# Optimization experiments

Measured on AMD Instinct MI355X. Metric: run time of the kernel, lower is better.

Reference implementation:

```python
import jax, jax.numpy as jnp
import numpy as np

N = 100000   # nodes
E = 3200000  # edges (avg degree 32)
F_IN = 128   # node feature dim (lazy in_channels)
C = 16       # GAT out_channels, heads=1
ED = 2       # edge_dim
B = 512      # graphs in batch
OUT_X = 64; OUT_Y = 64; ROT = 4
EPS = 1e-5


def _bn(x, g, b):
    # BatchNorm1d in training mode: biased batch variance, eps=1e-5
    mu = x.mean(0, keepdims=True)
    var = x.var(0, keepdims=True)
    return g * (x - mu) * jax.lax.rsqrt(var + EPS) + b


def _gat(x, src, dst, edge_attr, W, We, att_s, att_d, att_e, bias):
    # PyG GATConv, heads=1: self-loops added with fill_value='mean' edge attrs
    n = x.shape[0]
    deg = jax.ops.segment_sum(jnp.ones_like(dst, jnp.float32), dst, num_segments=n)
    loop_attr = jax.ops.segment_sum(edge_attr, dst, num_segments=n) / jnp.maximum(deg, 1.0)[:, None]
    idx = jnp.arange(n)
    src_f = jnp.concatenate([src, idx])
    dst_f = jnp.concatenate([dst, idx])
    ea = jnp.concatenate([edge_attr, loop_attr], axis=0)  # [E+N, ED]
    h = x @ W                      # [N, C]
    a_s = h @ att_s                # [N]
    a_d = h @ att_d                # [N]
    a_e = (ea @ We) @ att_e        # [E+N]
    logits = jax.nn.leaky_relu(a_s[src_f] + a_d[dst_f] + a_e, 0.2)
    m = jax.ops.segment_max(logits, dst_f, num_segments=n)  # every node has a self-loop
    ex = jnp.exp(logits - m[dst_f])
    alpha = ex / jax.ops.segment_sum(ex, dst_f, num_segments=n)[dst_f]
    return jax.ops.segment_sum(alpha[:, None] * h[src_f], dst_f, num_segments=n) + bias


def _glorot(k, shp):
    lim = float(np.sqrt(6.0 / (shp[0] + shp[1])))
    return jax.random.uniform(k, shp, jnp.float32, -lim, lim)


def setup_inputs() -> dict:
    key = jax.random.key(0)
    k = jax.random.split(key, 48)
    d = {}
    d['x'] = jax.random.normal(k[0], (N, F_IN), jnp.float32)
    d['edge_index'] = jax.random.randint(k[1], (2, E), 0, N)
    d['edge_attr'] = jax.random.normal(k[2], (E, ED), jnp.float32)
    d['batch'] = jnp.sort(jax.random.randint(k[3], (N,), 0, B))
    # gat1
    d['W1'] = _glorot(k[4], (F_IN, C)); d['We1'] = _glorot(k[5], (ED, C))
    d['as1'] = 0.1 * jax.random.normal(k[6], (C,)); d['ad1'] = 0.1 * jax.random.normal(k[7], (C,))
    d['ae1'] = 0.1 * jax.random.normal(k[8], (C,)); d['b1'] = jnp.zeros((C,), jnp.float32)
    # norm1 (BatchNorm on nodes)
    d['g1'] = 1.0 + 0.1 * jax.random.normal(k[9], (C,)); d['bb1'] = 0.1 * jax.random.normal(k[10], (C,))
    # gat2
    d['W2'] = _glorot(k[11], (C, C)); d['We2'] = _glorot(k[12], (ED, C))
    d['as2'] = 0.1 * jax.random.normal(k[13], (C,)); d['ad2'] = 0.1 * jax.random.normal(k[14], (C,))
    d['ae2'] = 0.1 * jax.random.normal(k[15], (C,)); d['b2'] = jnp.zeros((C,), jnp.float32)
    # D2RL MLP tail
    d['gL1'] = 1.0 + 0.1 * jax.random.normal(k[16], (C,)); d['bL1'] = 0.1 * jax.random.normal(k[17], (C,))
    d['Wl1'] = _glorot(k[18], (C, C)); d['bl1'] = 0.1 * jax.random.normal(k[19], (C,))
    d['gL2'] = 1.0 + 0.1 * jax.random.normal(k[20], (2 * C,)); d['bL2'] = 0.1 * jax.random.normal(k[21], (2 * C,))
    d['Wl2'] = _glorot(k[22], (2 * C, C)); d['bl2'] = 0.1 * jax.random.normal(k[23], (C,))
    d['gL3'] = 1.0 + 0.1 * jax.random.normal(k[24], (2 * C,)); d['bL3'] = 0.1 * jax.random.normal(k[25], (2 * C,))
    d['Wl3'] = _glorot(k[26], (2 * C, C)); d['bl3'] = 0.1 * jax.random.normal(k[27], (C,))
    d['Wx'] = _glorot(k[28], (C, OUT_X)); d['bx'] = 0.1 * jax.random.normal(k[29], (OUT_X,))
    d['Wy'] = _glorot(k[30], (C, OUT_Y)); d['by'] = 0.1 * jax.random.normal(k[31], (OUT_Y,))
    d['Wr'] = _glorot(k[32], (C, ROT)); d['br'] = 0.1 * jax.random.normal(k[33], (ROT,))
    return d


def reference(x, edge_index, edge_attr, batch,
              W1, We1, as1, ad1, ae1, b1, g1, bb1,
              W2, We2, as2, ad2, ae2, b2,
              gL1, bL1, Wl1, bl1, gL2, bL2, Wl2, bl2, gL3, bL3, Wl3, bl3,
              Wx, bx, Wy, by, Wr, br):
    src, dst = edge_index[0], edge_index[1]
    h = jax.nn.relu(_gat(x, src, dst, edge_attr, W1, We1, as1, ad1, ae1, b1))
    h = _bn(h, g1, bb1)
    h = jax.nn.relu(_gat(h, src, dst, edge_attr, W2, We2, as2, ad2, ae2, b2))
    # MeanAggregation over graphs
    cnt = jax.ops.segment_sum(jnp.ones((h.shape[0],), jnp.float32), batch, num_segments=B)
    xe = jax.ops.segment_sum(h, batch, num_segments=B) / jnp.maximum(cnt, 1.0)[:, None]  # [B, C]
    z = _bn(xe, gL1, bL1)
    z = jax.nn.relu(z @ Wl1 + bl1)
    z = _bn(jnp.concatenate([z, xe], axis=1), gL2, bL2)
    z = jax.nn.relu(z @ Wl2 + bl2)
    z = _bn(jnp.concatenate([z, xe], axis=1), gL3, bL3)
    z = jax.nn.relu(z @ Wl3 + bl3)
    xx = jax.nn.softmax(z @ Wx + bx, axis=1)
    y = jax.nn.softmax(z @ Wy + by, axis=1)
    rot = jax.nn.softmax(z @ Wr + br, axis=1)
    return (xx, y, rot)
```

## Files before the change

kernel.cpp:

```cpp
#include <hip/hip_runtime.h>
#include <hip/hip_fp16.h>
#include <math.h>

#define C 16
#define FIN 128

typedef unsigned int u32x2 __attribute__((ext_vector_type(2)));

__global__ __launch_bounds__(256) void k_gemm1(
    const float* __restrict__ x, const float* __restrict__ W,
    const float* __restrict__ asw, const float* __restrict__ adw,
    __half* __restrict__ hh, float* __restrict__ a_s, float* __restrict__ a_d, int n) {
  __shared__ float xs[64 * 129];
  __shared__ float Ws[FIN * C];
  __shared__ float pAs[4][64], pAd[4][64];
  int t = threadIdx.x;
  int node0 = blockIdx.x * 64;
  for (int i = t; i < FIN * C; i += 256) Ws[i] = W[i];
  for (int i = t; i < 64 * FIN; i += 256) {
    int r = i >> 7, c = i & 127;
    int node = node0 + r;
    xs[r * 129 + c] = (node < n) ? x[(size_t)node * FIN + c] : 0.f;
  }
  __syncthreads();
  int nn = t & 63, cg = (t >> 6) * 4, grp = t >> 6;
  float a0 = 0.f, a1 = 0.f, a2 = 0.f, a3 = 0.f;
  const float* xr = &xs[nn * 129];
  #pragma unroll 8
  for (int k = 0; k < FIN; ++k) {
    float xv = xr[k];
    const float* wr = &Ws[k * C + cg];
    a0 += xv * wr[0]; a1 += xv * wr[1]; a2 += xv * wr[2]; a3 += xv * wr[3];
  }
  int node = node0 + nn;
  if (node < n) {
    __half2 p0 = __floats2half2_rn(a0, a1), p1 = __floats2half2_rn(a2, a3);
    unsigned u0, u1;
    memcpy(&u0, &p0, 4); memcpy(&u1, &p1, 4);
    *(uint2*)(hh + (size_t)node * 16 + cg) = make_uint2(u0, u1);
  }
  pAs[grp][nn] = a0 * asw[cg] + a1 * asw[cg + 1] + a2 * asw[cg + 2] + a3 * asw[cg + 3];
  pAd[grp][nn] = a0 * adw[cg] + a1 * adw[cg + 1] + a2 * adw[cg + 2] + a3 * adw[cg + 3];
  __syncthreads();
  if (t < 64 && node0 + t < n) {
    a_s[node0 + t] = pAs[0][t] + pAs[1][t] + pAs[2][t] + pAs[3][t];
    a_d[node0 + t] = pAd[0][t] + pAd[1][t] + pAd[2][t] + pAd[3][t];
  }
}

__global__ __launch_bounds__(512) void k_scan1(const int* __restrict__ counts,
                                               int* __restrict__ bsum, int n) {
  __shared__ int sd[512];
  int i = blockIdx.x * 512 + threadIdx.x;
  sd[threadIdx.x] = (i < n) ? counts[i] : 0;
  __syncthreads();
  for (int s = 256; s > 0; s >>= 1) {
    if (threadIdx.x < s) sd[threadIdx.x] += sd[threadIdx.x + s];
    __syncthreads();
  }
  if (threadIdx.x == 0) bsum[blockIdx.x] = sd[0];
}

__global__ __launch_bounds__(512) void k_scan2(int* __restrict__ bsum,
                                               int* __restrict__ offs,
                                               int nblk, int n) {
  __shared__ int sd[512];
  int t = threadIdx.x;
  int v = (t < nblk) ? bsum[t] : 0;
  sd[t] = v;
  __syncthreads();
  for (int off = 1; off < 512; off <<= 1) {
    int x = (t >= off) ? sd[t - off] : 0;
    __syncthreads();
    sd[t] += x;
    __syncthreads();
  }
  if (t < nblk) bsum[t] = sd[t] - v;
  if (t == nblk - 1) offs[n] = sd[t];
}

__global__ __launch_bounds__(512) void k_scan3(const int* __restrict__ counts,
                                               const int* __restrict__ bsum,
                                               int* __restrict__ offs, int n) {
  __shared__ int sd[512];
  int t = threadIdx.x;
  int i = blockIdx.x * 512 + t;
  int v = (i < n) ? counts[i] : 0;
  sd[t] = v;
  __syncthreads();
  for (int off = 1; off < 512; off <<= 1) {
    int x = (t >= off) ? sd[t - off] : 0;
    __syncthreads();
    sd[t] += x;
    __syncthreads();
  }
  if (i < n) offs[i] = bsum[blockIdx.x] + sd[t] - v;
}


__global__ __launch_bounds__(256) void k_p1count(
    const int* __restrict__ dst, int* __restrict__ histT,
    int ne, int chunk, int G, int nbin) {
  __shared__ int hist[512];
  int g = blockIdx.x, t = threadIdx.x;
  for (int i = t; i < nbin; i += 256) hist[i] = 0;
  __syncthreads();
  int e0 = g * chunk, e1 = e0 + chunk; if (e1 > ne) e1 = ne;
  for (int e = e0 + t; e < e1; e += 256) atomicAdd(&hist[dst[e] >> 8], 1);
  __syncthreads();
  for (int i = t; i < nbin; i += 256) histT[i * G + g] = hist[i];
}

__global__ __launch_bounds__(256) void k_p1scat(
    const int* __restrict__ src, const int* __restrict__ dst,
    const float2* __restrict__ ea, const int* __restrict__ histS,
    const float* __restrict__ We1, const float* __restrict__ ae1,
    const float* __restrict__ We2, const float* __restrict__ ae2,
    uint2* __restrict__ tmpR, int* __restrict__ tmpD,
    int ne, int chunk, int G, int nbin) {
  __shared__ int cur[512];
  int g = blockIdx.x, t = threadIdx.x;
  for (int i = t; i < nbin; i += 256) cur[i] = histS[i * G + g];
  float w01 = 0.f, w11 = 0.f, w02 = 0.f, w12 = 0.f;
  #pragma unroll
  for (int c = 0; c < C; ++c) {
    w01 += We1[c] * ae1[c]; w11 += We1[C + c] * ae1[c];
    w02 += We2[c] * ae2[c]; w12 += We2[C + c] * ae2[c];
  }
  __syncthreads();
  int e0 = g * chunk, e1 = e0 + chunk; if (e1 > ne) e1 = ne;
  for (int e = e0 + t; e < e1; e += 256) {
    int d = dst[e];
    int pos = atomicAdd(&cur[d >> 8], 1);
    float2 a = ea[e];
    __half2 hp = __floats2half2_rn(a.x * w01 + a.y * w11, a.x * w02 + a.y * w12);
    unsigned hb;
    memcpy(&hb, &hp, 4);
    tmpR[pos] = make_uint2((unsigned)src[e], hb);
    tmpD[pos] = d;
  }
}

__global__ __launch_bounds__(256) void k_p2(
    const uint2* __restrict__ tmpR, const int* __restrict__ tmpD,
    const int* __restrict__ histS,
    uint2* __restrict__ bucket, int* __restrict__ offs,
    int G, int nbin, int n, int ne) {
  __shared__ int hist[256], scn[256], cur[256];
  int b = blockIdx.x, t = threadIdx.x;
  int cs0 = histS[b * G];
  int cs1 = (b + 1 < nbin) ? histS[(b + 1) * G] : ne;
  hist[t] = 0;
  __syncthreads();
  for (int i = cs0 + t; i < cs1; i += 256) atomicAdd(&hist[tmpD[i] & 255], 1);
  __syncthreads();
  int v = hist[t];
  scn[t] = v;
  __syncthreads();
  for (int off = 1; off < 256; off <<= 1) {
    int x = (t >= off) ? scn[t - off] : 0;
    __syncthreads();
    scn[t] += x;
    __syncthreads();
  }
  int excl = scn[t] - v;
  int node = b * 256 + t;
  if (node <= n) offs[node] = cs0 + excl;
  if (b == 0 && t == 0) offs[n] = ne;
  cur[t] = cs0 + excl;
  __syncthreads();
  for (int i = cs0 + t; i < cs1; i += 256) {
    int d = tmpD[i];
    int pos = atomicAdd(&cur[d & 255], 1);
    bucket[pos] = tmpR[i];
  }
}

__global__ __launch_bounds__(256) void k_hist_rank(
    const int* __restrict__ dst, int* __restrict__ counts,
    int* __restrict__ rank, int ne) {
  int e = blockIdx.x * 256 + threadIdx.x;
  if (e < ne) rank[e] = atomicAdd(&counts[dst[e]], 1);
}

__global__ __launch_bounds__(256) void k_scatter(
    const int* __restrict__ src, const int* __restrict__ dst,
    const float2* __restrict__ ea, const int* __restrict__ offs,
    const int* __restrict__ rank,
    const float* __restrict__ We1, const float* __restrict__ ae1,
    const float* __restrict__ We2, const float* __restrict__ ae2,
    uint2* __restrict__ bucket, int ne) {
  int e = blockIdx.x * 256 + threadIdx.x;
  if (e >= ne) return;
  float w01 = 0.f, w11 = 0.f, w02 = 0.f, w12 = 0.f;
  #pragma unroll
  for (int c = 0; c < C; ++c) {
    w01 += We1[c] * ae1[c]; w11 += We1[C + c] * ae1[c];
    w02 += We2[c] * ae2[c]; w12 += We2[C + c] * ae2[c];
  }
  int d = dst[e];
  float2 a = ea[e];
  __half2 hp = __floats2half2_rn(a.x * w01 + a.y * w11, a.x * w02 + a.y * w12);
  unsigned hb;
  memcpy(&hb, &hp, 4);
  bucket[offs[d] + rank[e]] = make_uint2((unsigned)src[e], hb);
}

__global__ __launch_bounds__(256) void k_gather(
    const uint2* __restrict__ bucket, const int* __restrict__ offs,
    const float* __restrict__ a_s, const float* __restrict__ a_d,
    const __half* __restrict__ hh, const float* __restrict__ bias,
    float* __restrict__ outv, float* __restrict__ bnsum, float* __restrict__ bnsq,
    int lay, int do_bn, int n) {
  __shared__ float sbn[32];
  int t = threadIdx.x;
  if (do_bn) {
    if (t < 32) sbn[t] = 0.f;
    __syncthreads();
  }

  int node = blockIdx.x * 64 + (t >> 2);
  int l = t & 3, f = l & 1, p = l >> 1;

  float acc[8];
  #pragma unroll
  for (int j = 0; j < 8; ++j) acc[j] = 0.f;
  float den = 0.f, ssum = 0.f;
  int o0 = 0, o1 = 0;
  float adi = 0.f, asi = 0.f;
  if (node < n) {
    o0 = offs[node]; o1 = offs[node + 1];
    adi = a_d[node]; asi = a_s[node];
    int e = o0 + p;
    u32x2 r = {0u, 0u};
    if (e < o1) r = __builtin_nontemporal_load((const u32x2*)(bucket + e));
    while (e < o1) {
      int en = e + 2;
      u32x2 rn = {0u, 0u};
      if (en < o1) rn = __builtin_nontemporal_load((const u32x2*)(bucket + en));
      int s = (int)r.x;
      unsigned scb = r.y;
      __half2 sc2;
      memcpy(&sc2, &scb, 4);
      float se = lay ? __high2float(sc2) : __low2float(sc2);
      float asv = a_s[s];
      uint4 hv = *(const uint4*)(hh + ((size_t)s << 4) + (f << 3));
      float lg = asv + adi + se;
      lg = lg > 0.f ? lg : 0.2f * lg;
      float ex = __expf(lg);
      den += ex; ssum += se;
      __half2 t0, t1, t2, t3;
      memcpy(&t0, &hv.x, 4); memcpy(&t1, &hv.y, 4);
      memcpy(&t2, &hv.z, 4); memcpy(&t3, &hv.w, 4);
      float2 g0 = __half22float2(t0), g1 = __half22float2(t1);
      float2 g2 = __half22float2(t2), g3 = __half22float2(t3);
      acc[0] += ex * g0.x; acc[1] += ex * g0.y;
      acc[2] += ex * g1.x; acc[3] += ex * g1.y;
      acc[4] += ex * g2.x; acc[5] += ex * g2.y;
      acc[6] += ex * g3.x; acc[7] += ex * g3.y;
      r = rn; e = en;
    }
  }
  den += __shfl_xor(den, 2);
  ssum += __shfl_xor(ssum, 2);
  #pragma unroll
  for (int j = 0; j < 8; ++j) acc[j] += __shfl_xor(acc[j], 2);

  float v[8];
  #pragma unroll
  for (int j = 0; j < 8; ++j) v[j] = 0.f;
  if (node < n) {
    float dgc = fmaxf((float)(o1 - o0), 1.f);
    float lg = asi + adi + ssum / dgc;
    lg = lg > 0.f ? lg : 0.2f * lg;
    float exs = __expf(lg);
    uint4 hv = *(const uint4*)(hh + ((size_t)node << 4) + (f << 3));
    __half2 t0, t1, t2, t3;
    memcpy(&t0, &hv.x, 4); memcpy(&t1, &hv.y, 4);
    memcpy(&t2, &hv.z, 4); memcpy(&t3, &hv.w, 4);
    float2 g0 = __half22float2(t0), g1 = __half22float2(t1);
    float2 g2 = __half22float2(t2), g3 = __half22float2(t3);
    float hs[8] = {g0.x, g0.y, g1.x, g1.y, g2.x, g2.y, g3.x, g3.y};
    float inv = 1.f / (den + exs);
    const float* bp = bias + f * 8;
    #pragma unroll
    for (int j = 0; j < 8; ++j)
      v[j] = fmaxf((acc[j] + exs * hs[j]) * inv + bp[j], 0.f);
    if (p == 0) {
      float4* op = (float4*)(outv + ((size_t)node << 4));
      op[f * 2]     = make_float4(v[0], v[1], v[2], v[3]);
      op[f * 2 + 1] = make_float4(v[4], v[5], v[6], v[7]);
    }
  }

  if (do_bn) {
    float sv[8], qv[8];
    bool act = (node < n) && (p == 0);
    #pragma unroll
    for (int j = 0; j < 8; ++j) {
      sv[j] = act ? v[j] : 0.f;
      qv[j] = sv[j] * sv[j];
    }
    #pragma unroll
    for (int j = 0; j < 8; ++j) {
      sv[j] += __shfl_down(sv[j], 4);  qv[j] += __shfl_down(qv[j], 4);
      sv[j] += __shfl_down(sv[j], 8);  qv[j] += __shfl_down(qv[j], 8);
      sv[j] += __shfl_down(sv[j], 16); qv[j] += __shfl_down(qv[j], 16);
      sv[j] += __shfl_down(sv[j], 32); qv[j] += __shfl_down(qv[j], 32);
    }
    if ((t & 63) < 2) {
      #pragma unroll
      for (int j = 0; j < 8; ++j) {
        atomicAdd(&sbn[f * 8 + j], sv[j]);
        atomicAdd(&sbn[16 + f * 8 + j], qv[j]);
      }
    }
    __syncthreads();
    if (t < 16) atomicAdd(&bnsum[t], sbn[t]);
    else if (t < 32) atomicAdd(&bnsq[t - 16], sbn[t]);
  }
}

__global__ void k_bnp(const float* __restrict__ bnsum, const float* __restrict__ bnsq,
                      const float* __restrict__ g, const float* __restrict__ bb,
                      float* __restrict__ scale, float* __restrict__ shift, float invn) {
  int c = threadIdx.x;
  if (c >= C) return;
  float mean = bnsum[c] * invn;
  float var = bnsq[c] * invn - mean * mean;
  float s = g[c] * rsqrtf(var + 1e-5f);
  scale[c] = s; shift[c] = bb[c] - mean * s;
}

__global__ __launch_bounds__(256) void k_node2(
    const float* __restrict__ outv, const float* __restrict__ scale,
    const float* __restrict__ shift, const float* __restrict__ W2,
    const float* __restrict__ asw, const float* __restrict__ adw,
    __half* __restrict__ hh, float* __restrict__ a_s, float* __restrict__ a_d, int n) {
  __shared__ float w2s[C * C];
  if (threadIdx.x < C * C) w2s[threadIdx.x] = W2[threadIdx.x];
  __syncthreads();
  int i = blockIdx.x * 256 + threadIdx.x;
  if (i >= n) return;
  float hn[C];
  #pragma unroll
  for (int c = 0; c < C; ++c) hn[c] = outv[(size_t)i * C + c] * scale[c] + shift[c];
  float h2[C];
  #pragma unroll
  for (int j = 0; j < C; ++j) {
    float acc = 0.f;
    #pragma unroll
    for (int c = 0; c < C; ++c) acc += hn[c] * w2s[c * C + j];
    h2[j] = acc;
  }
  float hs = 0.f, hd = 0.f;
  #pragma unroll
  for (int j = 0; j < C; ++j) { hs += h2[j] * asw[j]; hd += h2[j] * adw[j]; }
  a_s[i] = hs; a_d[i] = hd;
  unsigned wbits[8];
  #pragma unroll
  for (int j = 0; j < 8; ++j) {
    __half2 hq = __floats2half2_rn(h2[2 * j], h2[2 * j + 1]);
    memcpy(&wbits[j], &hq, 4);
  }
  uint4* hp = (uint4*)(hh + (size_t)i * 16);
  hp[0] = make_uint4(wbits[0], wbits[1], wbits[2], wbits[3]);
  hp[1] = make_uint4(wbits[4], wbits[5], wbits[6], wbits[7]);
}

__global__ void k_gstart(const int* __restrict__ batch, int* __restrict__ gs,
                         int n, int B_) {
  int g = blockIdx.x * blockDim.x + threadIdx.x;
  if (g > B_) return;
  if (g == B_) { gs[B_] = n; return; }
  int lo = 0, hi = n;
  while (lo < hi) { int mid = (lo + hi) >> 1; if (batch[mid] < g) lo = mid + 1; else hi = mid; }
  gs[g] = lo;
}

__global__ __launch_bounds__(256) void k_xe(
    const float* __restrict__ outv, const int* __restrict__ gs,
    float* __restrict__ xe, int B_) {
  int wave = blockIdx.x * 4 + (threadIdx.x >> 6);
  if (wave >= B_) return;
  int lane = threadIdx.x & 63;
  int c = lane & 15, sub = lane >> 4;
  int base = gs[wave], end = gs[wave + 1];
  float s = 0.f;
  for (int n0 = base + sub; n0 < end; n0 += 4) s += outv[(size_t)n0 * C + c];
  s += __shfl_down(s, 32);
  s += __shfl_down(s, 16);
  if (lane < 16) xe[(size_t)wave * C + c] = s / fmaxf((float)(end - base), 1.f);
}

__global__ __launch_bounds__(512) void k_tail_z3(
    const float* __restrict__ xe_in,
    const float* __restrict__ gL1, const float* __restrict__ bL1,
    const float* __restrict__ Wl1, const float* __restrict__ bl1,
    const float* __restrict__ gL2, const float* __restrict__ bL2,
    const float* __restrict__ Wl2, const float* __restrict__ bl2,
    const float* __restrict__ gL3, const float* __restrict__ bL3,
    const float* __restrict__ Wl3, const float* __restrict__ bl3,
    float* __restrict__ z3buf, int B_) {
  __shared__ float ssum[2 * C], ssq[2 * C], sc[2 * C], sh[2 * C];
  int t = threadIdx.x;
  float invB = 1.f / (float)B_;
  float xe[C];
  #pragma unroll
  for (int c = 0; c < C; ++c) xe[c] = xe_in[(size_t)t * C + c];

  if (t < 2 * C) { ssum[t] = 0.f; ssq[t] = 0.f; }
  __syncthreads();
  #pragma unroll
  for (int c = 0; c < C; ++c) {
    float s = xe[c], q = xe[c] * xe[c];
    for (int o = 32; o > 0; o >>= 1) { s += __shfl_down(s, o); q += __shfl_down(q, o); }
    if ((t & 63) == 0) { atomicAdd(&ssum[c], s); atomicAdd(&ssq[c], q); }
  }
  __syncthreads();
  if (t < C) {
    float mean = ssum[t] * invB, var = ssq[t] * invB - mean * mean;
    float s = gL1[t] * rsqrtf(var + 1e-5f);
    sc[t] = s; sh[t] = bL1[t] - mean * s;
  }
  __syncthreads();
  float z[C];
  #pragma unroll
  for (int j = 0; j < C; ++j) {
    float acc = bl1[j];
    #pragma unroll
    for (int c = 0; c < C; ++c) acc += (xe[c] * sc[c] + sh[c]) * Wl1[c * C + j];
    z[j] = fmaxf(acc, 0.f);
  }
  __syncthreads();

  if (t < 2 * C) { ssum[t] = 0.f; ssq[t] = 0.f; }
  __syncthreads();
  #pragma unroll
  for (int c = 0; c < C; ++c) {
    float s = z[c], q = z[c] * z[c];
    for (int o = 32; o > 0; o >>= 1) { s += __shfl_down(s, o); q += __shfl_down(q, o); }
    if ((t & 63) == 0) { atomicAdd(&ssum[c], s); atomicAdd(&ssq[c], q); }
    float s2 = xe[c], q2 = xe[c] * xe[c];
    for (int o = 32; o > 0; o >>= 1) { s2 += __shfl_down(s2, o); q2 += __shfl_down(q2, o); }
    if ((t & 63) == 0) { atomicAdd(&ssum[C + c], s2); atomicAdd(&ssq[C + c], q2); }
  }
  __syncthreads();
  if (t < 2 * C) {
    float mean = ssum[t] * invB, var = ssq[t] * invB - mean * mean;
    float s = gL2[t] * rsqrtf(var + 1e-5f);
    sc[t] = s; sh[t] = bL2[t] - mean * s;
  }
  __syncthreads();
  float z2[C];
  #pragma unroll
  for (int j = 0; j < C; ++j) {
    float acc = bl2[j];
    #pragma unroll
    for (int c = 0; c < C; ++c) acc += (z[c] * sc[c] + sh[c]) * Wl2[c * C + j];
    #pragma unroll
    for (int c = 0; c < C; ++c) acc += (xe[c] * sc[C + c] + sh[C + c]) * Wl2[(C + c) * C + j];
    z2[j] = fmaxf(acc, 0.f);
  }
  __syncthreads();

  if (t < 2 * C) { ssum[t] = 0.f; ssq[t] = 0.f; }
  __syncthreads();
  #pragma unroll
  for (int c = 0; c < C; ++c) {
    float s = z2[c], q = z2[c] * z2[c];
    for (int o = 32; o > 0; o >>= 1) { s += __shfl_down(s, o); q += __shfl_down(q, o); }
    if ((t & 63) == 0) { atomicAdd(&ssum[c], s); atomicAdd(&ssq[c], q); }
    float s2 = xe[c], q2 = xe[c] * xe[c];
    for (int o = 32; o > 0; o >>= 1) { s2 += __shfl_down(s2, o); q2 += __shfl_down(q2, o); }
    if ((t & 63) == 0) { atomicAdd(&ssum[C + c], s2); atomicAdd(&ssq[C + c], q2); }
  }
  __syncthreads();
  if (t < 2 * C) {
    float mean = ssum[t] * invB, var = ssq[t] * invB - mean * mean;
    float s = gL3[t] * rsqrtf(var + 1e-5f);
    sc[t] = s; sh[t] = bL3[t] - mean * s;
  }
  __syncthreads();
  #pragma unroll
  for (int j = 0; j < C; ++j) {
    float acc = bl3[j];
    #pragma unroll
    for (int c = 0; c < C; ++c) acc += (z2[c] * sc[c] + sh[c]) * Wl3[c * C + j];
    #pragma unroll
    for (int c = 0; c < C; ++c) acc += (xe[c] * sc[C + c] + sh[C + c]) * Wl3[(C + c) * C + j];
    z3buf[(size_t)t * C + j] = fmaxf(acc, 0.f);
  }
}

__global__ __launch_bounds__(256) void k_heads(
    const float* __restrict__ z3buf,
    const float* __restrict__ Wx, const float* __restrict__ bx,
    const float* __restrict__ Wy, const float* __restrict__ by,
    const float* __restrict__ Wr, const float* __restrict__ br,
    float* __restrict__ out, int B_) {
  int wv = blockIdx.x * 4 + (threadIdx.x >> 6);
  if (wv >= B_) return;
  int lane = threadIdx.x & 63;
  float z[C];
  #pragma unroll
  for (int c = 0; c < C; ++c) z[c] = z3buf[(size_t)wv * C + c];

  float ax = bx[lane];
  #pragma unroll
  for (int c = 0; c < C; ++c) ax += z[c] * Wx[c * 64 + lane];
  float m = ax;
  #pragma unroll
  for (int o = 32; o > 0; o >>= 1) m = fmaxf(m, __shfl_xor(m, o));
  float e = __expf(ax - m);
  float s = e;
  #pragma unroll
  for (int o = 32; o > 0; o >>= 1) s += __shfl_xor(s, o);
  out[(size_t)wv * 64 + lane] = e / s;

  float ay = by[lane];
  #pragma unroll
  for (int c = 0; c < C; ++c) ay += z[c] * Wy[c * 64 + lane];
  m = ay;
  #pragma unroll
  for (int o = 32; o > 0; o >>= 1) m = fmaxf(m, __shfl_xor(m, o));
  e = __expf(ay - m);
  s = e;
  #pragma unroll
  for (int o = 32; o > 0; o >>= 1) s += __shfl_xor(s, o);
  out[(size_t)B_ * 64 + (size_t)wv * 64 + lane] = e / s;

  if (lane < 4) {
    float ar = br[lane];
    #pragma unroll
    for (int c = 0; c < C; ++c) ar += z[c] * Wr[c * 4 + lane];
    float mr = ar;
    mr = fmaxf(mr, __shfl_xor(mr, 1));
    mr = fmaxf(mr, __shfl_xor(mr, 2));
    float er = __expf(ar - mr);
    float sr = er;
    sr += __shfl_xor(sr, 1);
    sr += __shfl_xor(sr, 2);
    out[(size_t)B_ * 128 + (size_t)wv * 4 + lane] = er / sr;
  }
}

extern "C" void kernel_launch(void* const* d_in, const int* in_sizes, int n_in,
                              void* d_out, int out_size, void* d_ws, size_t ws_size,
                              hipStream_t stream) {
  const float* x     = (const float*)d_in[0];
  const int*   eidx  = (const int*)d_in[1];
  const float* eattr = (const float*)d_in[2];
  const int*   batch = (const int*)d_in[3];
  const float* W1  = (const float*)d_in[4];
  const float* We1 = (const float*)d_in[5];
  const float* as1 = (const float*)d_in[6];
  const float* ad1 = (const float*)d_in[7];
  const float* ae1 = (const float*)d_in[8];
  const float* b1  = (const float*)d_in[9];
  const float* g1  = (const float*)d_in[10];
  const float* bb1 = (const float*)d_in[11];
  const float* W2  = (const float*)d_in[12];
  const float* We2 = (const float*)d_in[13];
  const float* as2 = (const float*)d_in[14];
  const float* ad2 = (const float*)d_in[15];
  const float* ae2 = (const float*)d_in[16];
  const float* b2  = (const float*)d_in[17];
  const float* gL1 = (const float*)d_in[18];
  const float* bL1 = (const float*)d_in[19];
  const float* Wl1 = (const float*)d_in[20];
  const float* bl1 = (const float*)d_in[21];
  const float* gL2 = (const float*)d_in[22];
  const float* bL2 = (const float*)d_in[23];
  const float* Wl2 = (const float*)d_in[24];
  const float* bl2 = (const float*)d_in[25];
  const float* gL3 = (const float*)d_in[26];
  const float* bL3 = (const float*)d_in[27];
  const float* Wl3 = (const float*)d_in[28];
  const float* bl3 = (const float*)d_in[29];
  const float* Wx  = (const float*)d_in[30];
  const float* bx  = (const float*)d_in[31];
  const float* Wy  = (const float*)d_in[32];
  const float* by  = (const float*)d_in[33];
  const float* Wr  = (const float*)d_in[34];
  const float* br  = (const float*)d_in[35];

  int N = in_sizes[3];
  int E = in_sizes[2] / 2;
  int B = out_size / 132;

  const int* src = eidx;
  const int* dst = eidx + E;

  const int G = 256;
  int nbin = (N + 255) >> 8;
  int nscan = nbin * G;
  int chunk = (E + G - 1) / G;
  int nblk2 = (nscan + 511) / 512;

  char* w = (char*)d_ws;
  size_t o = 0;
  auto alloc = [&](size_t bytes) { char* p = w + o; o += (bytes + 15) & ~15ull; return p; };
  uint2*  bucket = (uint2*)alloc((size_t)E * 8);
  uint2*  tmpR   = (uint2*)alloc((size_t)E * 8);
  int*    tmpD   = (int*)alloc((size_t)E * 4);
  __half* hh     = (__half*)alloc((size_t)N * C * 2);
  float*  outv   = (float*)alloc((size_t)N * C * 4);
  float*  a_s    = (float*)alloc((size_t)N * 4);
  float*  a_d    = (float*)alloc((size_t)N * 4);
  int*    offs   = (int*)alloc((size_t)(N + 4) * 4);
  int*    histT  = (int*)alloc((size_t)(nscan + 4) * 4);
  int*    histS  = (int*)alloc((size_t)(nscan + 4) * 4);
  int*    bsum   = (int*)alloc((size_t)(nblk2 + 516) * 4);
  float*  bn     = (float*)alloc(64 * 4);
  float*  xe     = (float*)alloc((size_t)B * C * 4);
  int*    gs     = (int*)alloc((size_t)(B + 4) * 4);
  float*  z3buf  = (float*)alloc((size_t)B * C * 4);
  size_t need_radix = o;

  bool radix = (need_radix <= ws_size) && (nbin <= 512) && (nblk2 <= 512);

  hipMemsetAsync(bn, 0, 32 * 4, stream);
  k_gemm1<<<(N + 63) / 64, 256, 0, stream>>>(x, W1, as1, ad1, hh, a_s, a_d, N);

  if (radix) {
    k_p1count<<<G, 256, 0, stream>>>(dst, histT, E, chunk, G, nbin);
    k_scan1<<<nblk2, 512, 0, stream>>>(histT, bsum, nscan);
    k_scan2<<<1, 512, 0, stream>>>(bsum, histS, nblk2, nscan);
    k_scan3<<<nblk2, 512, 0, stream>>>(histT, bsum, histS, nscan);
    k_p1scat<<<G, 256, 0, stream>>>(src, dst, (const float2*)eattr, histS,
                                    We1, ae1, We2, ae2, tmpR, tmpD, E, chunk, G, nbin);
    k_p2<<<nbin, 256, 0, stream>>>(tmpR, tmpD, histS, bucket, offs, G, nbin, N, E);
  } else {
    int* rank   = (int*)tmpR;
    int* counts = (int*)tmpD;
    int nblk = (N + 511) / 512;
    int ebl = (E + 255) / 256;
    hipMemsetAsync(counts, 0, (size_t)N * 4, stream);
    k_hist_rank<<<ebl, 256, 0, stream>>>(dst, counts, rank, E);
    k_scan1<<<nblk, 512, 0, stream>>>(counts, bsum, N);
    k_scan2<<<1, 512, 0, stream>>>(bsum, offs, nblk, N);
    k_scan3<<<nblk, 512, 0, stream>>>(counts, bsum, offs, N);
    k_scatter<<<ebl, 256, 0, stream>>>(src, dst, (const float2*)eattr, offs, rank,
                                       We1, ae1, We2, ae2, bucket, E);
  }

  int nbl = (N + 255) / 256;
  k_gather<<<(N + 63) / 64, 256, 0, stream>>>(bucket, offs, a_s, a_d, hh, b1,
                                              outv, bn, bn + 16, 0, 1, N);
  k_bnp<<<1, 64, 0, stream>>>(bn, bn + 16, g1, bb1, bn + 32, bn + 48, 1.f / (float)N);
  k_node2<<<nbl, 256, 0, stream>>>(outv, bn + 32, bn + 48, W2, as2, ad2, hh, a_s, a_d, N);
  k_gather<<<(N + 63) / 64, 256, 0, stream>>>(bucket, offs, a_s, a_d, hh, b2,
                                              outv, bn, bn + 16, 1, 0, N);
  k_gstart<<<(B + 1 + 255) / 256, 256, 0, stream>>>(batch, gs, N, B);
  k_xe<<<(B + 3) / 4, 256, 0, stream>>>(outv, gs, xe, B);
  k_tail_z3<<<1, B, 0, stream>>>(xe, gL1, bL1, Wl1, bl1, gL2, bL2, Wl2, bl2,
                                 gL3, bL3, Wl3, bl3, z3buf, B);
  k_heads<<<(B + 3) / 4, 256, 0, stream>>>(z3buf, Wx, bx, Wy, by, Wr, br,
                                           (float*)d_out, B);
}
```

Baseline: 672.8 us.

## Pack low dst bits into src word to drop tmpD array in radix sort

The first radix pass now stores the low 8 bits of the destination in the top byte of the source index, so the separate tmpD array is no longer written or read. The second pass extracts the sub-bin from that packed word and masks it off before writing the bucket. Edge attribute and tmpR reads use nontemporal loads, and the number of first-pass blocks is halved from 256 to 128. This cuts edge-sized memory traffic, but it limits node count to 2^24 (guarded), and the fewer blocks may reduce parallelism in the count and scatter passes.

```diff
diff --git a/kernel.cpp b/kernel.cpp
--- a/kernel.cpp
+++ b/kernel.cpp
@@ -113,11 +113,10 @@
 
 __global__ __launch_bounds__(256) void k_p1scat(
     const int* __restrict__ src, const int* __restrict__ dst,
-    const float2* __restrict__ ea, const int* __restrict__ histS,
+    const float* __restrict__ ea, const int* __restrict__ histS,
     const float* __restrict__ We1, const float* __restrict__ ae1,
     const float* __restrict__ We2, const float* __restrict__ ae2,
-    uint2* __restrict__ tmpR, int* __restrict__ tmpD,
-    int ne, int chunk, int G, int nbin) {
+    uint2* __restrict__ tmpR, int ne, int chunk, int G, int nbin) {
   __shared__ int cur[512];
   int g = blockIdx.x, t = threadIdx.x;
   for (int i = t; i < nbin; i += 256) cur[i] = histS[i * G + g];
@@ -132,18 +131,18 @@
   for (int e = e0 + t; e < e1; e += 256) {
     int d = dst[e];
     int pos = atomicAdd(&cur[d >> 8], 1);
-    float2 a = ea[e];
-    __half2 hp = __floats2half2_rn(a.x * w01 + a.y * w11, a.x * w02 + a.y * w12);
+    u32x2 ab = __builtin_nontemporal_load((const u32x2*)(ea + 2 * (size_t)e));
+    float ax = __uint_as_float(ab.x);
+    float ay = __uint_as_float(ab.y);
+    __half2 hp = __floats2half2_rn(ax * w01 + ay * w11, ax * w02 + ay * w12);
     unsigned hb;
     memcpy(&hb, &hp, 4);
-    tmpR[pos] = make_uint2((unsigned)src[e], hb);
-    tmpD[pos] = d;
+    tmpR[pos] = make_uint2((unsigned)src[e] | ((unsigned)(d & 255) << 24), hb);
   }
 }
 
 __global__ __launch_bounds__(256) void k_p2(
-    const uint2* __restrict__ tmpR, const int* __restrict__ tmpD,
-    const int* __restrict__ histS,
+    const uint2* __restrict__ tmpR, const int* __restrict__ histS,
     uint2* __restrict__ bucket, int* __restrict__ offs,
     int G, int nbin, int n, int ne) {
   __shared__ int hist[256], scn[256], cur[256];
@@ -152,7 +151,10 @@
   int cs1 = (b + 1 < nbin) ? histS[(b + 1) * G] : ne;
   hist[t] = 0;
   __syncthreads();
-  for (int i = cs0 + t; i < cs1; i += 256) atomicAdd(&hist[tmpD[i] & 255], 1);
+  for (int i = cs0 + t; i < cs1; i += 256) {
+    u32x2 r = __builtin_nontemporal_load((const u32x2*)(tmpR + i));
+    atomicAdd(&hist[r.x >> 24], 1);
+  }
   __syncthreads();
   int v = hist[t];
   scn[t] = v;
@@ -170,9 +172,9 @@
   cur[t] = cs0 + excl;
   __syncthreads();
   for (int i = cs0 + t; i < cs1; i += 256) {
-    int d = tmpD[i];
-    int pos = atomicAdd(&cur[d & 255], 1);
-    bucket[pos] = tmpR[i];
+    u32x2 r = __builtin_nontemporal_load((const u32x2*)(tmpR + i));
+    int pos = atomicAdd(&cur[r.x >> 24], 1);
+    bucket[pos] = make_uint2(r.x & 0x00FFFFFFu, r.y);
   }
 }
 
@@ -592,7 +594,7 @@
   const int* src = eidx;
   const int* dst = eidx + E;
 
-  const int G = 256;
+  const int G = 128;
   int nbin = (N + 255) >> 8;
   int nscan = nbin * G;
   int chunk = (E + G - 1) / G;
@@ -603,11 +605,11 @@
   auto alloc = [&](size_t bytes) { char* p = w + o; o += (bytes + 15) & ~15ull; return p; };
   uint2*  bucket = (uint2*)alloc((size_t)E * 8);
   uint2*  tmpR   = (uint2*)alloc((size_t)E * 8);
-  int*    tmpD   = (int*)alloc((size_t)E * 4);
   __half* hh     = (__half*)alloc((size_t)N * C * 2);
   float*  outv   = (float*)alloc((size_t)N * C * 4);
   float*  a_s    = (float*)alloc((size_t)N * 4);
   float*  a_d    = (float*)alloc((size_t)N * 4);
+  int*    counts = (int*)alloc((size_t)(N + 4) * 4);
   int*    offs   = (int*)alloc((size_t)(N + 4) * 4);
   int*    histT  = (int*)alloc((size_t)(nscan + 4) * 4);
   int*    histS  = (int*)alloc((size_t)(nscan + 4) * 4);
@@ -616,9 +618,9 @@
   float*  xe     = (float*)alloc((size_t)B * C * 4);
   int*    gs     = (int*)alloc((size_t)(B + 4) * 4);
   float*  z3buf  = (float*)alloc((size_t)B * C * 4);
-  size_t need_radix = o;
-
-  bool radix = (need_radix <= ws_size) && (nbin <= 512) && (nblk2 <= 512);
+  size_t need = o;
+
+  bool radix = (need <= ws_size) && (nbin <= 512) && (nblk2 <= 512) && (N <= (1 << 24));
 
   hipMemsetAsync(bn, 0, 32 * 4, stream);
   k_gemm1<<<(N + 63) / 64, 256, 0, stream>>>(x, W1, as1, ad1, hh, a_s, a_d, N);
@@ -628,12 +630,11 @@
     k_scan1<<<nblk2, 512, 0, stream>>>(histT, bsum, nscan);
     k_scan2<<<1, 512, 0, stream>>>(bsum, histS, nblk2, nscan);
     k_scan3<<<nblk2, 512, 0, stream>>>(histT, bsum, histS, nscan);
-    k_p1scat<<<G, 256, 0, stream>>>(src, dst, (const float2*)eattr, histS,
-                                    We1, ae1, We2, ae2, tmpR, tmpD, E, chunk, G, nbin);
-    k_p2<<<nbin, 256, 0, stream>>>(tmpR, tmpD, histS, bucket, offs, G, nbin, N, E);
+    k_p1scat<<<G, 256, 0, stream>>>(src, dst, eattr, histS,
+                                    We1, ae1, We2, ae2, tmpR, E, chunk, G, nbin);
+    k_p2<<<nbin, 256, 0, stream>>>(tmpR, histS, bucket, offs, G, nbin, N, E);
   } else {
-    int* rank   = (int*)tmpR;
-    int* counts = (int*)tmpD;
+    int* rank = (int*)tmpR;
     int nblk = (N + 511) / 512;
     int ebl = (E + 255) / 256;
     hipMemsetAsync(counts, 0, (size_t)N * 4, stream);
```

After: 689.6 us. 1.02x slower.
